# Performance work log

Measured on AMD Instinct MI355X. Metric: run time of the kernel, lower is better.

Reference implementation:

```python
import jax, jax.numpy as jnp
import numpy as np

S = 14
L_COORD = 5.0
L_NOOBJ = 0.5


def setup_inputs() -> dict:
    key = jax.random.key(0)
    k1, k2, k3 = jax.random.split(key, 3)
    B = 4096
    pred = jax.random.uniform(k1, (B, S, S, 30), dtype=jnp.float32)
    target = jax.random.uniform(k2, (B, S, S, 30), dtype=jnp.float32)
    # matching real YOLO targets where most cells are background.
    gate = jax.random.uniform(k3, (B, S, S))
    conf = jnp.where(gate > 0.85, target[..., 4], 0.0)
    target = target.at[..., 4].set(conf)
    return {"pred_tensor": pred, "target_tensor": target}


def _to_xyxy(b):
    # b: (..., 5) [x, y, w, h, c] -> (..., 4) [x1, y1, x2, y2]
    c = b[..., :2] / 14.0
    half = 0.5 * b[..., 2:4]
    return jnp.concatenate([c - half, c + half], axis=-1)


def _iou_2v1(pbox, tbox):
    # pbox: (B,S,S,2,4) xyxy, tbox: (B,S,S,4) -> iou (B,S,S,2)
    lt = jnp.maximum(pbox[..., :2], tbox[..., None, :2])
    rb = jnp.minimum(pbox[..., 2:], tbox[..., None, 2:])
    wh = jnp.clip(rb - lt, 0.0)
    inter = wh[..., 0] * wh[..., 1]
    a1 = (pbox[..., 2] - pbox[..., 0]) * (pbox[..., 3] - pbox[..., 1])
    a2 = (tbox[..., 2] - tbox[..., 0]) * (tbox[..., 3] - tbox[..., 1])
    return inter / (a1 + a2[..., None] - inter)


def reference(pred_tensor, target_tensor):
    pred, target = pred_tensor, target_tensor
    N = pred.shape[0]
    dt = pred.dtype
    coo = (target[..., 4] > 0).astype(dt)          # (B,S,S) object cells
    noo = 1.0 - coo                                # background cells

    # no-object confidence loss over both conf slots (indices 4 and 9)
    noobj_loss = jnp.sum(noo * ((pred[..., 4] - target[..., 4]) ** 2
                                + (pred[..., 9] - target[..., 9]) ** 2))

    # boxes: (B,S,S,2,5)
    pb = pred[..., :10].reshape(pred.shape[0], S, S, 2, 5)
    tb = target[..., :10].reshape(target.shape[0], S, S, 2, 5)

    # IoU of both predicted boxes vs first target box; detached (torch uses .data)
    iou = jax.lax.stop_gradient(_iou_2v1(_to_xyxy(pb), _to_xyxy(tb[..., 0, :])))
    resp = jax.nn.one_hot(jnp.argmax(iou, axis=-1), 2, dtype=dt)  # (B,S,S,2)
    max_iou = jnp.max(iou, axis=-1)                               # (B,S,S)

    p_resp = jnp.einsum('bijk,bijkc->bijc', resp, pb)  # responsible pred box
    t_resp = jnp.einsum('bijk,bijkc->bijc', resp, tb)  # matching target box
    conf_not_resp = jnp.einsum('bijk,bijk->bij', 1.0 - resp, pb[..., 4])

    contain_loss = jnp.sum(coo * (p_resp[..., 4] - max_iou) ** 2)
    not_contain_loss = jnp.sum(coo * conf_not_resp ** 2)  # target conf forced to 0

    loc_loss = jnp.sum(coo[..., None] * ((p_resp[..., :2] - t_resp[..., :2]) ** 2
               + (jnp.sqrt(p_resp[..., 2:4]) - jnp.sqrt(t_resp[..., 2:4])) ** 2))

    class_loss = jnp.sum(coo[..., None] * (pred[..., 10:] - target[..., 10:]) ** 2)

    total = (L_COORD * loc_loss + contain_loss
             + L_NOOBJ * (noobj_loss + not_contain_loss) + class_loss) / N
    return total
```

## Files before the change

### kernel.cpp

```cpp
#include <hip/hip_runtime.h>


__device__ __forceinline__ float cell_loss(const float* __restrict__ p,
                                           const float* __restrict__ t)
{
    const bool coo = t[4] > 0.0f;
    if (!coo) {
        float d4 = p[4] - t[4];
        float d9 = p[9] - t[9];
        return 0.5f * (d4 * d4 + d9 * d9);
    }
    const float inv14 = 1.0f / 14.0f;
    float p0x1 = p[0]*inv14 - 0.5f*p[2], p0y1 = p[1]*inv14 - 0.5f*p[3];
    float p0x2 = p[0]*inv14 + 0.5f*p[2], p0y2 = p[1]*inv14 + 0.5f*p[3];
    float p1x1 = p[5]*inv14 - 0.5f*p[7], p1y1 = p[6]*inv14 - 0.5f*p[8];
    float p1x2 = p[5]*inv14 + 0.5f*p[7], p1y2 = p[6]*inv14 + 0.5f*p[8];
    float tx1  = t[0]*inv14 - 0.5f*t[2], ty1  = t[1]*inv14 - 0.5f*t[3];
    float tx2  = t[0]*inv14 + 0.5f*t[2], ty2  = t[1]*inv14 + 0.5f*t[3];

    float at = (tx2 - tx1) * (ty2 - ty1);

    float w0 = fmaxf(fminf(p0x2, tx2) - fmaxf(p0x1, tx1), 0.0f);
    float h0 = fmaxf(fminf(p0y2, ty2) - fmaxf(p0y1, ty1), 0.0f);
    float inter0 = w0 * h0;
    float a0 = (p0x2 - p0x1) * (p0y2 - p0y1);
    float iou0 = inter0 / (a0 + at - inter0);

    float w1 = fmaxf(fminf(p1x2, tx2) - fmaxf(p1x1, tx1), 0.0f);
    float h1 = fmaxf(fminf(p1y2, ty2) - fmaxf(p1y1, ty1), 0.0f);
    float inter1 = w1 * h1;
    float a1 = (p1x2 - p1x1) * (p1y2 - p1y1);
    float iou1 = inter1 / (a1 + at - inter1);

    bool  r1      = iou1 > iou0;
    float max_iou = fmaxf(iou0, iou1);

    float prx = r1 ? p[5] : p[0], pry = r1 ? p[6] : p[1];
    float prw = r1 ? p[7] : p[2], prh = r1 ? p[8] : p[3];
    float prc = r1 ? p[9] : p[4];
    float trx = r1 ? t[5] : t[0], try_ = r1 ? t[6] : t[1];
    float trw = r1 ? t[7] : t[2], trh = r1 ? t[8] : t[3];
    float cnr = r1 ? p[4] : p[9];

    float dc = prc - max_iou;
    float contain = dc * dc;
    float not_contain = cnr * cnr;

    float dx = prx - trx, dy = pry - try_;
    float dw = sqrtf(prw) - sqrtf(trw);
    float dh = sqrtf(prh) - sqrtf(trh);
    float loc = dx * dx + dy * dy + dw * dw + dh * dh;

    float cls = 0.0f;
#pragma unroll
    for (int k = 10; k < 30; ++k) {
        float d = p[k] - t[k];
        cls += d * d;
    }
    return 5.0f * loc + contain + 0.5f * not_contain + cls;
}

__global__ __launch_bounds__(256) void yolo_cells(
    const float* __restrict__ pred, const float* __restrict__ targ,
    float* __restrict__ partial, int npairs)
{
    float acc = 0.0f;
    const int pair = blockIdx.x * 256 + threadIdx.x;
    if (pair < npairs) {
        float p[60], t[60];
        const float4* P4 = reinterpret_cast<const float4*>(pred) + (size_t)pair * 15;
        const float4* T4 = reinterpret_cast<const float4*>(targ) + (size_t)pair * 15;
#pragma unroll
        for (int i = 0; i < 15; ++i) {
            float4 v = P4[i];
            p[4*i+0] = v.x; p[4*i+1] = v.y; p[4*i+2] = v.z; p[4*i+3] = v.w;
        }
#pragma unroll
        for (int i = 0; i < 15; ++i) {
            float4 v = T4[i];
            t[4*i+0] = v.x; t[4*i+1] = v.y; t[4*i+2] = v.z; t[4*i+3] = v.w;
        }
        asm volatile("" ::: "memory");

        acc  = cell_loss(p,      t);
        acc += cell_loss(p + 30, t + 30);
    }

    __shared__ float sm[256];
    sm[threadIdx.x] = acc;
    __syncthreads();
#pragma unroll
    for (int s = 128; s > 0; s >>= 1) {
        if (threadIdx.x < s) sm[threadIdx.x] += sm[threadIdx.x + s];
        __syncthreads();
    }
    if (threadIdx.x == 0) partial[blockIdx.x] = sm[0];
}

__global__ __launch_bounds__(256) void yolo_final(
    const float* __restrict__ partial, int n, float* __restrict__ out, float invN)
{
    __shared__ float sm[256];
    float acc = 0.0f;
    for (int i = threadIdx.x; i < n; i += 256) acc += partial[i];
    sm[threadIdx.x] = acc;
    __syncthreads();
#pragma unroll
    for (int s = 128; s > 0; s >>= 1) {
        if (threadIdx.x < s) sm[threadIdx.x] += sm[threadIdx.x + s];
        __syncthreads();
    }
    if (threadIdx.x == 0) out[0] = sm[0] * invN;
}

extern "C" void kernel_launch(void* const* d_in, const int* in_sizes, int n_in,
                              void* d_out, int out_size, void* d_ws, size_t ws_size,
                              hipStream_t stream) {
    const float* pred = (const float*)d_in[0];
    const float* targ = (const float*)d_in[1];
    float* out = (float*)d_out;
    float* partial = (float*)d_ws;

    const int ncells = in_sizes[0] / 30;
    const int B      = ncells / 196;
    const float invN = 1.0f / (float)B;

    const int npairs = ncells / 2;
    const int nblocks = (npairs + 255) / 256;

    yolo_cells<<<nblocks, 256, 0, stream>>>(pred, targ, partial, npairs);
    yolo_final<<<1, 256, 0, stream>>>(partial, nblocks, out, invN);
}
```

Before: 38.10 us.

## Stage cells through shared memory with coalesced loads in a persistent grid-stride loop

Each block now loads a 256-cell tile of pred and target with fully coalesced float4 accesses into LDS, then each thread computes one cell's loss from shared memory. The grid is capped at 512 persistent blocks that loop over tiles, prefetching the next tile into registers while computing the current one. This replaces strided per-thread 240-byte loads, which coalesce poorly, and overlaps global loads with compute. In exchange it uses 60KB of LDS per block, which limits occupancy, and reading per-cell strides of 30 floats from LDS causes bank conflicts.

```diff
diff --git a/kernel.cpp b/kernel.cpp
--- a/kernel.cpp
+++ b/kernel.cpp
@@ -1,5 +1,10 @@
 #include <hip/hip_runtime.h>
 
+
+#define TPB 256
+#define CPT 256
+#define F4T (CPT * 30 / 4)
+#define NBLOCKS 512
 
 __device__ __forceinline__ float cell_loss(const float* __restrict__ p,
                                            const float* __restrict__ t)
@@ -60,41 +65,70 @@
     return 5.0f * loc + contain + 0.5f * not_contain + cls;
 }
 
-__global__ __launch_bounds__(256) void yolo_cells(
+__global__ __launch_bounds__(TPB) void yolo_cells(
     const float* __restrict__ pred, const float* __restrict__ targ,
-    float* __restrict__ partial, int npairs)
+    float* __restrict__ partial, int ncells)
 {
+    __shared__ float smem[CPT * 60];
+    float4* smem4 = reinterpret_cast<float4*>(smem);
+    const float4* P4 = reinterpret_cast<const float4*>(pred);
+    const float4* T4 = reinterpret_cast<const float4*>(targ);
+
+    const int ntiles = (ncells + CPT - 1) / CPT;
+    const long maxf4 = (long)ncells * 30 / 4 - 1;
+    const int tid = threadIdx.x;
     float acc = 0.0f;
-    const int pair = blockIdx.x * 256 + threadIdx.x;
-    if (pair < npairs) {
-        float p[60], t[60];
-        const float4* P4 = reinterpret_cast<const float4*>(pred) + (size_t)pair * 15;
-        const float4* T4 = reinterpret_cast<const float4*>(targ) + (size_t)pair * 15;
+
+    float4 reg[15];
+    int tile = blockIdx.x;
+
+    if (tile < ntiles) {
 #pragma unroll
         for (int i = 0; i < 15; ++i) {
-            float4 v = P4[i];
-            p[4*i+0] = v.x; p[4*i+1] = v.y; p[4*i+2] = v.z; p[4*i+3] = v.w;
+            int j = i * TPB + tid;
+            bool isP = j < F4T;
+            long g = (long)tile * F4T + (isP ? j : j - F4T);
+            if (g > maxf4) g = maxf4;
+            reg[i] = isP ? P4[g] : T4[g];
         }
-#pragma unroll
-        for (int i = 0; i < 15; ++i) {
-            float4 v = T4[i];
-            t[4*i+0] = v.x; t[4*i+1] = v.y; t[4*i+2] = v.z; t[4*i+3] = v.w;
-        }
-        asm volatile("" ::: "memory");
-
-        acc  = cell_loss(p,      t);
-        acc += cell_loss(p + 30, t + 30);
     }
 
-    __shared__ float sm[256];
-    sm[threadIdx.x] = acc;
+    while (tile < ntiles) {
+        __syncthreads();
+#pragma unroll
+        for (int i = 0; i < 15; ++i) smem4[i * TPB + tid] = reg[i];
+        __syncthreads();
+
+        int next = tile + gridDim.x;
+        if (next < ntiles) {
+#pragma unroll
+            for (int i = 0; i < 15; ++i) {
+                int j = i * TPB + tid;
+                bool isP = j < F4T;
+                long g = (long)next * F4T + (isP ? j : j - F4T);
+                if (g > maxf4) g = maxf4;
+                reg[i] = isP ? P4[g] : T4[g];
+            }
+        }
+
+        int cell = tile * CPT + tid;
+        if (cell < ncells) {
+            const float* p = smem + tid * 30;
+            const float* t = smem + CPT * 30 + tid * 30;
+            acc += cell_loss(p, t);
+        }
+        tile = next;
+    }
+
+    __shared__ float red[TPB];
+    red[tid] = acc;
     __syncthreads();
 #pragma unroll
-    for (int s = 128; s > 0; s >>= 1) {
-        if (threadIdx.x < s) sm[threadIdx.x] += sm[threadIdx.x + s];
+    for (int s = TPB / 2; s > 0; s >>= 1) {
+        if (tid < s) red[tid] += red[tid + s];
         __syncthreads();
     }
-    if (threadIdx.x == 0) partial[blockIdx.x] = sm[0];
+    if (tid == 0) partial[blockIdx.x] = red[0];
 }
 
 __global__ __launch_bounds__(256) void yolo_final(
@@ -125,9 +159,9 @@
     const int B      = ncells / 196;
     const float invN = 1.0f / (float)B;
 
-    const int npairs = ncells / 2;
-    const int nblocks = (npairs + 255) / 256;
+    const int ntiles = (ncells + CPT - 1) / CPT;
+    const int nblocks = ntiles < NBLOCKS ? ntiles : NBLOCKS;
 
-    yolo_cells<<<nblocks, 256, 0, stream>>>(pred, targ, partial, npairs);
+    yolo_cells<<<nblocks, TPB, 0, stream>>>(pred, targ, partial, ncells);
     yolo_final<<<1, 256, 0, stream>>>(partial, nblocks, out, invN);
 }
```

New measurement: 93.16 us. 145% more time.

## Double-buffer cell tiles via direct global-to-LDS loads in persistent single-wave blocks

Applied to the files above, without the earlier changes.

Replaces the one-pair-per-thread register load with persistent 64-thread blocks that stream 64-cell tiles of pred and target straight into LDS using global_load_lds. Two buffers are used, so the next tile's loads overlap the current tile's loss computation, coordinated with manual vmcnt waits. The shared-memory tree reduction is replaced by a wavefront shuffle reduction. This aims to keep more memory traffic in flight and make loads fully coalesced. The risks are the hand-written waitcnt counting, LDS bank conflicts from the stride-30 per-lane reads, and limited parallelism from capping the grid at 1280 blocks.

```diff
diff --git a/kernel.cpp b/kernel.cpp
--- a/kernel.cpp
+++ b/kernel.cpp
@@ -1,5 +1,17 @@
 #include <hip/hip_runtime.h>
 
+
+#define CPW 64
+#define F4P 480
+#define F4C (2 * F4P)
+#define LPI 15
+#define MAXBLK 1280
+
+__device__ __forceinline__ void gload_lds16(const void* g, void* s) {
+    auto g1 = (const __attribute__((address_space(1))) void*)(uintptr_t)g;
+    auto s3 = (__attribute__((address_space(3))) void*)(uint32_t)(uintptr_t)s;
+    __builtin_amdgcn_global_load_lds(g1, s3, 16, 0, 0);
+}
 
 __device__ __forceinline__ float cell_loss(const float* __restrict__ p,
                                            const float* __restrict__ t)
@@ -60,41 +72,63 @@
     return 5.0f * loc + contain + 0.5f * not_contain + cls;
 }
 
-__global__ __launch_bounds__(256) void yolo_cells(
+__global__ __launch_bounds__(64) void yolo_cells(
     const float* __restrict__ pred, const float* __restrict__ targ,
-    float* __restrict__ partial, int npairs)
+    float* __restrict__ partial, int ncells)
 {
+    __shared__ float4 smem4[2][F4C];
+    const float4* P4 = reinterpret_cast<const float4*>(pred);
+    const float4* T4 = reinterpret_cast<const float4*>(targ);
+
+    const int  lane   = threadIdx.x;
+    const int  wtiles = (ncells + CPW - 1) / CPW;
+    const long maxf4  = (long)ncells * 30 / 4 - 1;
+
     float acc = 0.0f;
-    const int pair = blockIdx.x * 256 + threadIdx.x;
-    if (pair < npairs) {
-        float p[60], t[60];
-        const float4* P4 = reinterpret_cast<const float4*>(pred) + (size_t)pair * 15;
-        const float4* T4 = reinterpret_cast<const float4*>(targ) + (size_t)pair * 15;
+    int tile = blockIdx.x;
+
+    if (tile < wtiles) {
 #pragma unroll
-        for (int i = 0; i < 15; ++i) {
-            float4 v = P4[i];
-            p[4*i+0] = v.x; p[4*i+1] = v.y; p[4*i+2] = v.z; p[4*i+3] = v.w;
+        for (int i = 0; i < LPI; ++i) {
+            int  j   = i * 64 + lane;
+            bool isP = j < F4P;
+            long g   = (long)tile * F4P + (isP ? j : j - F4P);
+            if (g > maxf4) g = maxf4;
+            gload_lds16(isP ? (const void*)(P4 + g) : (const void*)(T4 + g),
+                        (void*)&smem4[0][i * 64]);
         }
-#pragma unroll
-        for (int i = 0; i < 15; ++i) {
-            float4 v = T4[i];
-            t[4*i+0] = v.x; t[4*i+1] = v.y; t[4*i+2] = v.z; t[4*i+3] = v.w;
-        }
-        asm volatile("" ::: "memory");
-
-        acc  = cell_loss(p,      t);
-        acc += cell_loss(p + 30, t + 30);
     }
 
-    __shared__ float sm[256];
-    sm[threadIdx.x] = acc;
-    __syncthreads();
+    int buf = 0;
+    for (; tile < wtiles; tile += gridDim.x) {
+        int next = tile + gridDim.x;
+        if (next < wtiles) {
 #pragma unroll
-    for (int s = 128; s > 0; s >>= 1) {
-        if (threadIdx.x < s) sm[threadIdx.x] += sm[threadIdx.x + s];
-        __syncthreads();
+            for (int i = 0; i < LPI; ++i) {
+                int  j   = i * 64 + lane;
+                bool isP = j < F4P;
+                long g   = (long)next * F4P + (isP ? j : j - F4P);
+                if (g > maxf4) g = maxf4;
+                gload_lds16(isP ? (const void*)(P4 + g) : (const void*)(T4 + g),
+                            (void*)&smem4[buf ^ 1][i * 64]);
+            }
+            asm volatile("s_waitcnt vmcnt(15)" ::: "memory");
+        } else {
+            asm volatile("s_waitcnt vmcnt(0)" ::: "memory");
+        }
+        __builtin_amdgcn_sched_barrier(0);
+
+        const float* base = reinterpret_cast<const float*>(&smem4[buf][0]);
+        int cell = tile * CPW + lane;
+        if (cell < ncells)
+            acc += cell_loss(base + lane * 30, base + F4P * 4 + lane * 30);
+        buf ^= 1;
     }
-    if (threadIdx.x == 0) partial[blockIdx.x] = sm[0];
+
+#pragma unroll
+    for (int off = 32; off > 0; off >>= 1)
+        acc += __shfl_down(acc, off, 64);
+    if (lane == 0) partial[blockIdx.x] = acc;
 }
 
 __global__ __launch_bounds__(256) void yolo_final(
@@ -125,9 +159,9 @@
     const int B      = ncells / 196;
     const float invN = 1.0f / (float)B;
 
-    const int npairs = ncells / 2;
-    const int nblocks = (npairs + 255) / 256;
+    const int wtiles  = (ncells + CPW - 1) / CPW;
+    const int nblocks = wtiles < MAXBLK ? wtiles : MAXBLK;
 
-    yolo_cells<<<nblocks, 256, 0, stream>>>(pred, targ, partial, npairs);
+    yolo_cells<<<nblocks, 64, 0, stream>>>(pred, targ, partial, ncells);
     yolo_final<<<1, 256, 0, stream>>>(partial, nblocks, out, invN);
 }
```

Result: faster. 37.13 us, median of 2 (-2.6%).
